# Optimization experiments

Hardware: AMD Instinct MI355X
Metric: run time of the kernel (lower is better)

## Reference

```python
import jax, jax.numpy as jnp
import numpy as np
import math

SR = 44100
FRAME = 256
K = 80
NB = 16
MIDI_LO, MIDI_HI = 21.0, 108.0


def setup_inputs() -> dict:
    key = jax.random.key(0)
    k0, k1 = jax.random.split(key)
    B = 8
    # fundamental frequencies spread over ~4 octaves of the piano range (55..880 Hz)
    f0 = 55.0 * 2.0 ** (jax.random.uniform(k0, (B,)) * 4.0)
    vel_norm = jax.random.uniform(k1, (B,), minval=0.2, maxval=1.0)
    inp = dict(
        f0=f0.astype(jnp.float32),
        vel_norm=vel_norm.astype(jnp.float32),
        log_B_slope=jnp.float32(-2.0),
        log_B_intercept=jnp.float32(-7.5),
        log_tau1=jnp.linspace(math.log(0.4), math.log(0.05), K).astype(jnp.float32),
        log_tau2=jnp.linspace(math.log(5.0), math.log(0.3), K).astype(jnp.float32),
        logit_a1=jnp.linspace(-1.4, 0.0, K).astype(jnp.float32),
        log_beat_hz=jnp.linspace(math.log(0.3), math.log(1.5), K).astype(jnp.float32),
        logit_beat_depth=jnp.full((K,), -1.7, jnp.float32),
        log_A0=(-jnp.log(jnp.arange(1, K + 1, dtype=jnp.float32)) * 0.7),
        harm_detune=jnp.zeros((K,), jnp.float32),
        noise_band_gain=jnp.zeros((NB,), jnp.float32),
        log_tau_noise=jnp.float32(math.log(0.05)),
        log_noise_level=jnp.float32(math.log(0.08)),
        pan_scale=jnp.float32(0.0),
        n_frames=256,
    )
    return inp


def reference(f0, vel_norm, log_B_slope, log_B_intercept, log_tau1, log_tau2,
              logit_a1, log_beat_hz, logit_beat_depth, log_A0, harm_detune,
              noise_band_gain, log_tau_noise, log_noise_level, pan_scale,
              n_frames):
    N = n_frames * FRAME                                   # total audio samples
    t = jnp.arange(N, dtype=jnp.float32) * jnp.float32(1.0 / SR)   # (N,)
    two_pi = jnp.float32(2.0 * math.pi)

    # --- inharmonicity coefficient B(midi) = exp(clamp(slope*m + intercept)) ---
    midi = 69.0 + 12.0 * jnp.log2(f0 / 440.0)
    midi_norm = (midi - MIDI_LO) / (MIDI_HI - MIDI_LO)
    B_inh = jnp.exp(jnp.clip(log_B_slope * midi_norm + log_B_intercept, -14.0, -4.0))  # (B,)

    # --- inharmonic partial frequencies f_k = f0 * k * sqrt(1 + B k^2) ---
    ks = jnp.arange(1, K + 1, dtype=jnp.float32)           # (K,)
    freqs = f0[:, None] * ks * jnp.sqrt(1.0 + B_inh[:, None] * ks ** 2)  # (B,K)
    freqs = freqs * (1.0 + harm_detune)                    # learned per-partial detune
    alive = (freqs < SR / 2).astype(jnp.float32)           # nyquist mask (B,K)

    # --- double-exponential decay envelope per partial ---
    tau1 = jnp.exp(log_tau1)
    tau2 = jnp.exp(log_tau2)
    a1 = jax.nn.sigmoid(logit_a1)
    env = (a1[:, None] * jnp.exp(-t / tau1[:, None])
           + (1.0 - a1[:, None]) * jnp.exp(-t / tau2[:, None]))        # (K,N)

    # --- beating modulation (two-string coupling) ---
    depth = jax.nn.sigmoid(logit_beat_depth)
    bhz = jnp.exp(log_beat_hz)
    beat = 1.0 + 0.5 * depth[:, None] * (jnp.cos(two_pi * bhz[:, None] * t) - 1.0)  # (K,N)

    # --- oscillator bank: amp * env * beat * sin(2 pi f t) ---
    amp = jnp.exp(log_A0)[None, :] * vel_norm[:, None] * alive          # (B,K)
    phase = two_pi * freqs[:, :, None] * t                              # (B,K,N)
    partials = (amp[:, :, None] * (env * beat)[None]) * jnp.sin(phase)  # (B,K,N)

    # --- stereo panning per partial (constant-power) ---
    pan_init = (jnp.arange(K, dtype=jnp.float32) / max(K - 1, 1) * 2.0 - 1.0) * 0.1
    pan = jnp.tanh(pan_init * jnp.exp(pan_scale))                       # (K,)
    gains = jnp.stack([jnp.sqrt(0.5 * (1.0 - pan)),
                       jnp.sqrt(0.5 * (1.0 + pan))])                    # (2,K)
    audio = jnp.einsum('bkn,ck->bcn', partials, gains)                  # (B,2,N)

    # --- attack noise: log-spaced band oscillators with fast exp decay ---
    nf = jnp.exp(jnp.linspace(math.log(200.0), math.log(20000.0), NB)).astype(jnp.float32)
    n_alive = (nf < SR / 2).astype(jnp.float32)
    band_g = jax.nn.softmax(noise_band_gain) * n_alive                  # (NB,)
    noise_osc = jnp.sin(two_pi * nf[:, None] * t)                       # (NB,N)
    noise_env = jnp.exp(-t / jnp.exp(log_tau_noise))                    # (N,)
    noise_sig = (band_g @ noise_osc) * noise_env                        # (N,)
    noise = jnp.exp(log_noise_level) * vel_norm[:, None] * noise_sig[None, :]  # (B,N)

    return audio + noise[:, None, :]                                    # (B,2,N)
```

## Files before the change

### kernel.cpp

```cpp
#include <hip/hip_runtime.h>
#include <math.h>


#define KMAX 128
#define NBMAX 32

#define C2PI_HI 6.28318548202514648f
#define C2PI_LO -1.7484556e-7f
#define INV2PI  0.15915494309189535f

__device__ __forceinline__ float nofuse(float x) {
    asm volatile("" : "+v"(x));
    return x;
}

__device__ __forceinline__ float sin_cw(float ph) {
    float q = rintf(ph * INV2PI);
    float r = fmaf(q, -C2PI_HI, ph);
    r = fmaf(q, -C2PI_LO, r);
    return __sinf(r);
}


__global__ void pr_precomp(const float* __restrict__ f0,
                           const float* __restrict__ vel,
                           const float* __restrict__ pslope,
                           const float* __restrict__ pinter,
                           const float* __restrict__ log_tau1,
                           const float* __restrict__ log_tau2,
                           const float* __restrict__ logit_a1,
                           const float* __restrict__ log_beat_hz,
                           const float* __restrict__ logit_beat_depth,
                           const float* __restrict__ log_A0,
                           const float* __restrict__ harm_detune,
                           const float* __restrict__ noise_band_gain,
                           const float* __restrict__ plog_tau_noise,
                           const float* __restrict__ plog_noise_level,
                           const float* __restrict__ ppan_scale,
                           float* __restrict__ ws, int B, int K, int NB) {
    const int tid = threadIdx.x;
    const float two_pi = C2PI_HI;
    const float slope = pslope[0], inter = pinter[0], pan_scale = ppan_scale[0];

    float4* pk4 = (float4*)ws;
    float4* keA = pk4 + (size_t)B * K;
    float4* keB = keA + K;
    float4* nz  = keB + K;
    float*  nl  = (float*)(nz + NB);

    for (int i = tid; i < B * K; i += blockDim.x) {
        int b = i / K, k = i % K;
        float f0b = f0[b];
        float kf = (float)(k + 1);
        float fr = f0b / 440.0f;
        float midi = 69.0f + 12.0f * (float)log2((double)fr);
        float mn = (midi - 21.0f) / 87.0f;
        float z = nofuse(slope * mn) + inter;
        z = fminf(fmaxf(z, -14.0f), -4.0f);
        float Binh = (float)exp((double)z);
        float kk  = kf * kf;
        float bk2 = nofuse(Binh * kk);
        float arg = nofuse(1.0f + bk2);
        float s3  = (float)sqrt((double)arg);
        float r0  = nofuse(f0b * kf);
        float r1  = nofuse(r0 * s3);
        float dt  = nofuse(1.0f + harm_detune[k]);
        float fq  = nofuse(r1 * dt);
        float alive = (fq < 22050.0f) ? 1.0f : 0.0f;
        float amp = (float)exp((double)log_A0[k]) * vel[b] * alive;
        int km1 = (K - 1) > 1 ? (K - 1) : 1;
        float a = (float)k / (float)km1;
        float pini = nofuse((a * 2.0f - 1.0f) * 0.1f);
        float pexp = (float)exp((double)pan_scale);
        float pan = (float)tanh((double)nofuse(pini * pexp));
        float gl = (float)sqrt((double)(0.5f * (1.0f - pan)));
        float gr = (float)sqrt((double)(0.5f * (1.0f + pan)));
        float pf = nofuse(two_pi * fq);
        pk4[i] = make_float4(pf, amp * gl, amp * gr, 0.0f);
    }
    for (int k = tid; k < K; k += blockDim.x) {
        float tau1 = (float)exp((double)log_tau1[k]);
        float tau2 = (float)exp((double)log_tau2[k]);
        float a1 = (float)(1.0 / (1.0 + exp(-(double)logit_a1[k])));
        float bhz = (float)exp((double)log_beat_hz[k]);
        float dep = (float)(1.0 / (1.0 + exp(-(double)logit_beat_depth[k])));
        keA[k] = make_float4(1.0f / tau1, 1.0f / tau2, a1, 1.0f - a1);
        keB[k] = make_float4(nofuse(two_pi * bhz), 0.5f * dep, 0.0f, 0.0f);
    }
    for (int j = tid; j < NB; j += blockDim.x) {
        float m = -1e30f;
        for (int q = 0; q < NB; ++q) m = fmaxf(m, noise_band_gain[q]);
        float ssum = 0.0f;
        for (int q = 0; q < NB; ++q)
            ssum += (float)exp((double)(noise_band_gain[q] - m));
        double start = log(200.0), stop = log(20000.0);
        double step = (stop - start) / (double)(NB - 1);
        float lin = (j == NB - 1) ? (float)stop : (float)(start + (double)j * step);
        float nf = (float)exp((double)lin);
        float na = (nf < 22050.0f) ? 1.0f : 0.0f;
        float bg = ((float)exp((double)(noise_band_gain[j] - m)) / ssum) * na;
        nz[j] = make_float4(nofuse(two_pi * nf), bg, 0.0f, 0.0f);
    }
    for (int b = tid; b < B; b += blockDim.x)
        nl[b] = (float)exp((double)plog_noise_level[0]) * vel[b];
    if (tid == 0) nl[B] = 1.0f / (float)exp((double)plog_tau_noise[0]);
}

template <int BT>
__global__ __launch_bounds__(128) void pr_synth(
    const float4* __restrict__ pk4, const float4* __restrict__ keA,
    const float4* __restrict__ keB, const float4* __restrict__ nz,
    const float* __restrict__ nlp, float* __restrict__ out,
    int B, int K, int NB, int N) {
    __shared__ float4 s_pk[BT * KMAX];
    __shared__ float4 s_keA[KMAX];
    __shared__ float4 s_keB[KMAX];
    __shared__ float4 s_nz[NBMAX];
    __shared__ float  s_nl[BT];
    __shared__ float  s_itn;

    const int tid = threadIdx.x;
    const int bOff = blockIdx.y * BT;

    for (int i = tid; i < BT * K; i += blockDim.x) {
        int bi = i / K, k = i - bi * K;
        int b = bOff + bi;
        s_pk[i] = (b < B) ? pk4[(size_t)b * K + k] : make_float4(0, 0, 0, 0);
    }
    for (int i = tid; i < K; i += blockDim.x) {
        s_keA[i] = keA[i];
        s_keB[i] = keB[i];
    }
    for (int i = tid; i < NB; i += blockDim.x) s_nz[i] = nz[i];
    for (int i = tid; i < BT; i += blockDim.x)
        s_nl[i] = (bOff + i < B) ? nlp[bOff + i] : 0.0f;
    if (tid == 0) s_itn = nlp[B];
    __syncthreads();

    const int n = blockIdx.x * blockDim.x + tid;
    if (n >= N) return;
    const float t = (float)n * (float)(1.0 / 44100.0);
    const float nt = -t;

    float accL[BT], accR[BT];
#pragma unroll
    for (int bi = 0; bi < BT; ++bi) { accL[bi] = 0.0f; accR[bi] = 0.0f; }

    for (int k = 0; k < K; ++k) {
        float4 ka = s_keA[k];
        float4 kb = s_keB[k];
        float e1 = __expf(nt * ka.x);
        float e2 = __expf(nt * ka.y);
        float env = ka.z * e1 + ka.w * e2;
        float beat = fmaf(kb.y, __cosf(kb.x * t) - 1.0f, 1.0f);
        float eb = env * beat;
#pragma unroll
        for (int bi = 0; bi < BT; ++bi) {
            float4 p = s_pk[bi * K + k];
            float ph = p.x * t;
            float q = rintf(ph * INV2PI);
            float r = fmaf(q, -C2PI_HI, ph);
            r = fmaf(q, -C2PI_LO, r);
            float sv = __sinf(r);
            float pp = eb * sv;
            accL[bi] = fmaf(p.y, pp, accL[bi]);
            accR[bi] = fmaf(p.z, pp, accR[bi]);
        }
    }

    float ns = 0.0f;
    for (int j = 0; j < NB; ++j) {
        float4 zj = s_nz[j];
        ns = fmaf(zj.y, sin_cw(zj.x * t), ns);
    }
    float nsv = ns * __expf(nt * s_itn);

#pragma unroll
    for (int bi = 0; bi < BT; ++bi) {
        int b = bOff + bi;
        if (b < B) {
            float nois = s_nl[bi] * nsv;
            out[((size_t)(b * 2 + 0)) * N + n] = accL[bi] + nois;
            out[((size_t)(b * 2 + 1)) * N + n] = accR[bi] + nois;
        }
    }
}

extern "C" void kernel_launch(void* const* d_in, const int* in_sizes, int n_in,
                              void* d_out, int out_size, void* d_ws, size_t ws_size,
                              hipStream_t stream) {
    const float* f0    = (const float*)d_in[0];
    const float* vel   = (const float*)d_in[1];
    const float* slope = (const float*)d_in[2];
    const float* inter = (const float*)d_in[3];
    const float* lt1   = (const float*)d_in[4];
    const float* lt2   = (const float*)d_in[5];
    const float* la1   = (const float*)d_in[6];
    const float* lbh   = (const float*)d_in[7];
    const float* lbd   = (const float*)d_in[8];
    const float* lA0   = (const float*)d_in[9];
    const float* hdet  = (const float*)d_in[10];
    const float* nbg   = (const float*)d_in[11];
    const float* ltn   = (const float*)d_in[12];
    const float* lnl   = (const float*)d_in[13];
    const float* pans  = (const float*)d_in[14];

    const int B  = in_sizes[0];
    const int K  = in_sizes[4];
    const int NB = in_sizes[11];
    const int N  = out_size / (2 * B);

    float* ws = (float*)d_ws;

    hipLaunchKernelGGL(pr_precomp, dim3(1), dim3(256), 0, stream,
                       f0, vel, slope, inter, lt1, lt2, la1, lbh, lbd, lA0,
                       hdet, nbg, ltn, lnl, pans, ws, B, K, NB);

    const float4* pk4 = (const float4*)ws;
    const float4* keA = pk4 + (size_t)B * K;
    const float4* keB = keA + K;
    const float4* nz  = keB + K;
    const float*  nlp = (const float*)(nz + NB);

    dim3 grid((N + 127) / 128, (B + 7) / 8);
    hipLaunchKernelGGL(pr_synth<8>, grid, dim3(128), 0, stream,
                       pk4, keA, keB, nz, nlp, (float*)d_out, B, K, NB, N);
}
```

Measured before the change: 126.0 us.

## Split partial sum over K chunks into separate partial and combine kernels

Splits the synthesis across four chunks of the K partials, launching a second grid dimension so each block handles one chunk and writes per-chunk partial sums to workspace. A new combine kernel sums the chunks, adds the attack noise and writes the output. Block size also goes from 128 to 256. The aim is more parallelism (more blocks to fill the GPU), paid for with extra global memory traffic for the partial buffers and an additional kernel launch. The new kernels assume B equals BT (8) and that the workspace is large enough past offset 16384.

```diff
diff --git a/kernel.cpp b/kernel.cpp
--- a/kernel.cpp
+++ b/kernel.cpp
@@ -4,6 +4,8 @@
 
 #define KMAX 128
 #define NBMAX 32
+#define NCH 4
+#define KCMAX 32
 
 #define C2PI_HI 6.28318548202514648f
 #define C2PI_LO -1.7484556e-7f
@@ -21,6 +23,7 @@
     return __sinf(r);
 }
 
+#define PART_OFF 16384
 
 __global__ void pr_precomp(const float* __restrict__ f0,
                            const float* __restrict__ vel,
@@ -107,34 +110,29 @@
 }
 
 template <int BT>
-__global__ __launch_bounds__(128) void pr_synth(
+__global__ __launch_bounds__(256) void pr_part(
     const float4* __restrict__ pk4, const float4* __restrict__ keA,
-    const float4* __restrict__ keB, const float4* __restrict__ nz,
-    const float* __restrict__ nlp, float* __restrict__ out,
-    int B, int K, int NB, int N) {
-    __shared__ float4 s_pk[BT * KMAX];
-    __shared__ float4 s_keA[KMAX];
-    __shared__ float4 s_keB[KMAX];
-    __shared__ float4 s_nz[NBMAX];
-    __shared__ float  s_nl[BT];
-    __shared__ float  s_itn;
+    const float4* __restrict__ keB, float* __restrict__ part,
+    int B, int K, int N) {
+    const int KC = (K + NCH - 1) / NCH;
+    const int c = blockIdx.y;
+    const int k0 = c * KC;
+    const int k1 = min(K, k0 + KC);
+    const int nk = k1 - k0;
+
+    __shared__ float4 s_pk[BT * KCMAX];
+    __shared__ float4 s_keA[KCMAX];
+    __shared__ float4 s_keB[KCMAX];
 
     const int tid = threadIdx.x;
-    const int bOff = blockIdx.y * BT;
-
-    for (int i = tid; i < BT * K; i += blockDim.x) {
-        int bi = i / K, k = i - bi * K;
-        int b = bOff + bi;
-        s_pk[i] = (b < B) ? pk4[(size_t)b * K + k] : make_float4(0, 0, 0, 0);
-    }
-    for (int i = tid; i < K; i += blockDim.x) {
-        s_keA[i] = keA[i];
-        s_keB[i] = keB[i];
-    }
-    for (int i = tid; i < NB; i += blockDim.x) s_nz[i] = nz[i];
-    for (int i = tid; i < BT; i += blockDim.x)
-        s_nl[i] = (bOff + i < B) ? nlp[bOff + i] : 0.0f;
-    if (tid == 0) s_itn = nlp[B];
+    for (int i = tid; i < BT * nk; i += blockDim.x) {
+        int bi = i / nk, kk = i - bi * nk;
+        s_pk[bi * KCMAX + kk] = pk4[(size_t)bi * K + k0 + kk];
+    }
+    for (int i = tid; i < nk; i += blockDim.x) {
+        s_keA[i] = keA[k0 + i];
+        s_keB[i] = keB[k0 + i];
+    }
     __syncthreads();
 
     const int n = blockIdx.x * blockDim.x + tid;
@@ -146,9 +144,9 @@
 #pragma unroll
     for (int bi = 0; bi < BT; ++bi) { accL[bi] = 0.0f; accR[bi] = 0.0f; }
 
-    for (int k = 0; k < K; ++k) {
-        float4 ka = s_keA[k];
-        float4 kb = s_keB[k];
+    for (int kk = 0; kk < nk; ++kk) {
+        float4 ka = s_keA[kk];
+        float4 kb = s_keB[kk];
         float e1 = __expf(nt * ka.x);
         float e2 = __expf(nt * ka.y);
         float env = ka.z * e1 + ka.w * e2;
@@ -156,7 +154,7 @@
         float eb = env * beat;
 #pragma unroll
         for (int bi = 0; bi < BT; ++bi) {
-            float4 p = s_pk[bi * K + k];
+            float4 p = s_pk[bi * KCMAX + kk];
             float ph = p.x * t;
             float q = rintf(ph * INV2PI);
             float r = fmaf(q, -C2PI_HI, ph);
@@ -168,21 +166,44 @@
         }
     }
 
+#pragma unroll
+    for (int bi = 0; bi < BT; ++bi) {
+        part[((size_t)(c * 2 * BT + bi * 2 + 0)) * N + n] = accL[bi];
+        part[((size_t)(c * 2 * BT + bi * 2 + 1)) * N + n] = accR[bi];
+    }
+}
+
+template <int BT>
+__global__ __launch_bounds__(256) void pr_comb(
+    const float* __restrict__ part, const float4* __restrict__ nz,
+    const float* __restrict__ nlp, float* __restrict__ out,
+    int B, int NB, int N) {
+    __shared__ float4 s_nz[NBMAX];
+    __shared__ float  s_nl[BT + 1];
+    const int tid = threadIdx.x;
+    for (int i = tid; i < NB; i += blockDim.x) s_nz[i] = nz[i];
+    for (int i = tid; i < BT + 1; i += blockDim.x) s_nl[i] = nlp[i];
+    __syncthreads();
+
+    const int n = blockIdx.x * blockDim.x + tid;
+    if (n >= N) return;
+    const float t = (float)n * (float)(1.0 / 44100.0);
+
     float ns = 0.0f;
     for (int j = 0; j < NB; ++j) {
         float4 zj = s_nz[j];
         ns = fmaf(zj.y, sin_cw(zj.x * t), ns);
     }
-    float nsv = ns * __expf(nt * s_itn);
-
-#pragma unroll
-    for (int bi = 0; bi < BT; ++bi) {
-        int b = bOff + bi;
-        if (b < B) {
-            float nois = s_nl[bi] * nsv;
-            out[((size_t)(b * 2 + 0)) * N + n] = accL[bi] + nois;
-            out[((size_t)(b * 2 + 1)) * N + n] = accR[bi] + nois;
-        }
+    float nsv = ns * __expf(-t * s_nl[BT]);
+
+#pragma unroll
+    for (int j = 0; j < 2 * BT; ++j) {
+        float s = part[(size_t)j * N + n];
+#pragma unroll
+        for (int c = 1; c < NCH; ++c)
+            s += part[((size_t)(c * 2 * BT + j)) * N + n];
+        float nois = s_nl[j >> 1] * nsv;
+        out[(size_t)j * N + n] = s + nois;
     }
 }
 
@@ -221,8 +242,13 @@
     const float4* keB = keA + K;
     const float4* nz  = keB + K;
     const float*  nlp = (const float*)(nz + NB);
-
-    dim3 grid((N + 127) / 128, (B + 7) / 8);
-    hipLaunchKernelGGL(pr_synth<8>, grid, dim3(128), 0, stream,
-                       pk4, keA, keB, nz, nlp, (float*)d_out, B, K, NB, N);
-}
+    float* part = ws + PART_OFF;
+
+    dim3 gridA((N + 255) / 256, NCH);
+    hipLaunchKernelGGL(pr_part<8>, gridA, dim3(256), 0, stream,
+                       pk4, keA, keB, part, B, K, N);
+
+    dim3 gridB((N + 255) / 256);
+    hipLaunchKernelGGL(pr_comb<8>, gridB, dim3(256), 0, stream,
+                       part, nz, nlp, (float*)d_out, B, NB, N);
+}
```

Result: faster. 120.8 us (-4.1%).

## Split partial loop across four wavefronts with shared-memory reduction; parallelize precompute per batch

Applied to the files above, without the earlier changes.

The synth kernel now assigns 64 samples per block and splits the K partials across four wavefronts. Each wavefront accumulates a partial sum, and the sums are combined through shared memory before the output is written. This is meant to raise occupancy and parallelism, since the old grid had only N/128 blocks of 128 threads, each looping over all K partials serially. The precompute kernel also now runs one block per batch entry instead of a single block. The cost is an extra barrier, shared-memory reduction traffic, and a noise computation that every wavefront repeats redundantly.

```diff
diff --git a/kernel.cpp b/kernel.cpp
--- a/kernel.cpp
+++ b/kernel.cpp
@@ -4,6 +4,7 @@
 
 #define KMAX 128
 #define NBMAX 32
+#define NCH 4
 
 #define C2PI_HI 6.28318548202514648f
 #define C2PI_LO -1.7484556e-7f
@@ -39,6 +40,7 @@
                            const float* __restrict__ ppan_scale,
                            float* __restrict__ ws, int B, int K, int NB) {
     const int tid = threadIdx.x;
+    const int b = blockIdx.x;
     const float two_pi = C2PI_HI;
     const float slope = pslope[0], inter = pinter[0], pan_scale = ppan_scale[0];
 
@@ -48,36 +50,39 @@
     float4* nz  = keB + K;
     float*  nl  = (float*)(nz + NB);
 
-    for (int i = tid; i < B * K; i += blockDim.x) {
-        int b = i / K, k = i % K;
+    {
         float f0b = f0[b];
-        float kf = (float)(k + 1);
         float fr = f0b / 440.0f;
         float midi = 69.0f + 12.0f * (float)log2((double)fr);
         float mn = (midi - 21.0f) / 87.0f;
         float z = nofuse(slope * mn) + inter;
         z = fminf(fmaxf(z, -14.0f), -4.0f);
         float Binh = (float)exp((double)z);
-        float kk  = kf * kf;
-        float bk2 = nofuse(Binh * kk);
-        float arg = nofuse(1.0f + bk2);
-        float s3  = (float)sqrt((double)arg);
-        float r0  = nofuse(f0b * kf);
-        float r1  = nofuse(r0 * s3);
-        float dt  = nofuse(1.0f + harm_detune[k]);
-        float fq  = nofuse(r1 * dt);
-        float alive = (fq < 22050.0f) ? 1.0f : 0.0f;
-        float amp = (float)exp((double)log_A0[k]) * vel[b] * alive;
+        float pexp = (float)exp((double)pan_scale);
         int km1 = (K - 1) > 1 ? (K - 1) : 1;
-        float a = (float)k / (float)km1;
-        float pini = nofuse((a * 2.0f - 1.0f) * 0.1f);
-        float pexp = (float)exp((double)pan_scale);
-        float pan = (float)tanh((double)nofuse(pini * pexp));
-        float gl = (float)sqrt((double)(0.5f * (1.0f - pan)));
-        float gr = (float)sqrt((double)(0.5f * (1.0f + pan)));
-        float pf = nofuse(two_pi * fq);
-        pk4[i] = make_float4(pf, amp * gl, amp * gr, 0.0f);
-    }
+        for (int k = tid; k < K; k += blockDim.x) {
+            float kf = (float)(k + 1);
+            float kk  = kf * kf;
+            float bk2 = nofuse(Binh * kk);
+            float arg = nofuse(1.0f + bk2);
+            float s3  = (float)sqrt((double)arg);
+            float r0  = nofuse(f0b * kf);
+            float r1  = nofuse(r0 * s3);
+            float dt  = nofuse(1.0f + harm_detune[k]);
+            float fq  = nofuse(r1 * dt);
+            float alive = (fq < 22050.0f) ? 1.0f : 0.0f;
+            float amp = (float)exp((double)log_A0[k]) * vel[b] * alive;
+            float a = (float)k / (float)km1;
+            float pini = nofuse((a * 2.0f - 1.0f) * 0.1f);
+            float pan = (float)tanh((double)nofuse(pini * pexp));
+            float gl = (float)sqrt((double)(0.5f * (1.0f - pan)));
+            float gr = (float)sqrt((double)(0.5f * (1.0f + pan)));
+            float pf = nofuse(two_pi * fq);
+            pk4[(size_t)b * K + k] = make_float4(pf, amp * gl, amp * gr, 0.0f);
+        }
+    }
+
+    if (b != 0) return;
     for (int k = tid; k < K; k += blockDim.x) {
         float tau1 = (float)exp((double)log_tau1[k]);
         float tau2 = (float)exp((double)log_tau2[k]);
@@ -101,13 +106,13 @@
         float bg = ((float)exp((double)(noise_band_gain[j] - m)) / ssum) * na;
         nz[j] = make_float4(nofuse(two_pi * nf), bg, 0.0f, 0.0f);
     }
-    for (int b = tid; b < B; b += blockDim.x)
-        nl[b] = (float)exp((double)plog_noise_level[0]) * vel[b];
+    for (int bb = tid; bb < B; bb += blockDim.x)
+        nl[bb] = (float)exp((double)plog_noise_level[0]) * vel[bb];
     if (tid == 0) nl[B] = 1.0f / (float)exp((double)plog_tau_noise[0]);
 }
 
 template <int BT>
-__global__ __launch_bounds__(128) void pr_synth(
+__global__ __launch_bounds__(256, 4) void pr_synth(
     const float4* __restrict__ pk4, const float4* __restrict__ keA,
     const float4* __restrict__ keB, const float4* __restrict__ nz,
     const float* __restrict__ nlp, float* __restrict__ out,
@@ -116,37 +121,36 @@
     __shared__ float4 s_keA[KMAX];
     __shared__ float4 s_keB[KMAX];
     __shared__ float4 s_nz[NBMAX];
-    __shared__ float  s_nl[BT];
-    __shared__ float  s_itn;
-
-    const int tid = threadIdx.x;
-    const int bOff = blockIdx.y * BT;
+    __shared__ float  s_red[NCH][64][2 * BT + 1];
+
+    const int tid  = threadIdx.x;
+    const int lane = tid & 63;
+    const int g    = tid >> 6;
 
     for (int i = tid; i < BT * K; i += blockDim.x) {
         int bi = i / K, k = i - bi * K;
-        int b = bOff + bi;
-        s_pk[i] = (b < B) ? pk4[(size_t)b * K + k] : make_float4(0, 0, 0, 0);
+        s_pk[bi * KMAX + k] =
+            (bi < B) ? pk4[(size_t)bi * K + k] : make_float4(0, 0, 0, 0);
     }
     for (int i = tid; i < K; i += blockDim.x) {
         s_keA[i] = keA[i];
         s_keB[i] = keB[i];
     }
     for (int i = tid; i < NB; i += blockDim.x) s_nz[i] = nz[i];
-    for (int i = tid; i < BT; i += blockDim.x)
-        s_nl[i] = (bOff + i < B) ? nlp[bOff + i] : 0.0f;
-    if (tid == 0) s_itn = nlp[B];
     __syncthreads();
 
-    const int n = blockIdx.x * blockDim.x + tid;
-    if (n >= N) return;
+    const int n = blockIdx.x * 64 + lane;
     const float t = (float)n * (float)(1.0 / 44100.0);
     const float nt = -t;
+    const int KC = (K + NCH - 1) / NCH;
+    const int k0 = g * KC;
+    const int k1 = min(K, k0 + KC);
 
     float accL[BT], accR[BT];
 #pragma unroll
     for (int bi = 0; bi < BT; ++bi) { accL[bi] = 0.0f; accR[bi] = 0.0f; }
 
-    for (int k = 0; k < K; ++k) {
+    for (int k = k0; k < k1; ++k) {
         float4 ka = s_keA[k];
         float4 kb = s_keB[k];
         float e1 = __expf(nt * ka.x);
@@ -156,7 +160,7 @@
         float eb = env * beat;
 #pragma unroll
         for (int bi = 0; bi < BT; ++bi) {
-            float4 p = s_pk[bi * K + k];
+            float4 p = s_pk[bi * KMAX + k];
             float ph = p.x * t;
             float q = rintf(ph * INV2PI);
             float r = fmaf(q, -C2PI_HI, ph);
@@ -168,20 +172,32 @@
         }
     }
 
+#pragma unroll
+    for (int bi = 0; bi < BT; ++bi) {
+        s_red[g][lane][2 * bi + 0] = accL[bi];
+        s_red[g][lane][2 * bi + 1] = accR[bi];
+    }
+    __syncthreads();
+
     float ns = 0.0f;
     for (int j = 0; j < NB; ++j) {
         float4 zj = s_nz[j];
         ns = fmaf(zj.y, sin_cw(zj.x * t), ns);
     }
-    float nsv = ns * __expf(nt * s_itn);
-
-#pragma unroll
-    for (int bi = 0; bi < BT; ++bi) {
-        int b = bOff + bi;
-        if (b < B) {
-            float nois = s_nl[bi] * nsv;
-            out[((size_t)(b * 2 + 0)) * N + n] = accL[bi] + nois;
-            out[((size_t)(b * 2 + 1)) * N + n] = accR[bi] + nois;
+    float nsv = ns * __expf(nt * nlp[B]);
+
+    const int JT = (2 * BT) / NCH;
+    if (n < N) {
+#pragma unroll
+        for (int jj = 0; jj < JT; ++jj) {
+            int j = g * JT + jj;
+            int b = j >> 1;
+            if (b >= B) continue;
+            float s = 0.0f;
+#pragma unroll
+            for (int c = 0; c < NCH; ++c) s += s_red[c][lane][j];
+            float nois = nlp[b] * nsv;
+            out[(size_t)j * N + n] = s + nois;
         }
     }
 }
@@ -212,7 +228,7 @@
 
     float* ws = (float*)d_ws;
 
-    hipLaunchKernelGGL(pr_precomp, dim3(1), dim3(256), 0, stream,
+    hipLaunchKernelGGL(pr_precomp, dim3(B), dim3(128), 0, stream,
                        f0, vel, slope, inter, lt1, lt2, la1, lbh, lbd, lA0,
                        hdet, nbg, ltn, lnl, pans, ws, B, K, NB);
 
@@ -222,7 +238,7 @@
     const float4* nz  = keB + K;
     const float*  nlp = (const float*)(nz + NB);
 
-    dim3 grid((N + 127) / 128, (B + 7) / 8);
-    hipLaunchKernelGGL(pr_synth<8>, grid, dim3(128), 0, stream,
+    dim3 grid((N + 63) / 64);
+    hipLaunchKernelGGL(pr_synth<8>, grid, dim3(256), 0, stream,
                        pk4, keA, keB, nz, nlp, (float*)d_out, B, K, NB, N);
 }
```

After: 110.2 us. -12.6%, faster.
